# Kernel optimization log

Hardware: AMD Instinct MI355X
Metric: run time of the kernel (lower is better)

## Reference

```python
import jax, jax.numpy as jnp
import numpy as np

B, T, D = 4, 2048, 1024
H = 16
HD = D // H  # 64


def setup_inputs() -> dict:
    key = jax.random.key(0)
    ks = jax.random.split(key, 9)
    x = jax.random.normal(ks[0], (B, T, D), dtype=jnp.float32)
    s = 0.02
    Wq = jax.random.normal(ks[1], (D, D), dtype=jnp.float32) * s
    bq = jnp.zeros((D,), dtype=jnp.float32)
    Wk = jax.random.normal(ks[2], (D, D), dtype=jnp.float32) * s
    bk = jnp.zeros((D,), dtype=jnp.float32)
    Wv = jax.random.normal(ks[3], (D, D), dtype=jnp.float32) * s
    bv = jnp.zeros((D,), dtype=jnp.float32)
    Wo = jax.random.normal(ks[4], (D, D), dtype=jnp.float32) * s
    bo = jnp.zeros((D,), dtype=jnp.float32)
    return {"x": x, "Wq": Wq, "bq": bq, "Wk": Wk, "bk": bk,
            "Wv": Wv, "bv": bv, "Wo": Wo, "bo": bo}


def reference(x, Wq, bq, Wk, bk, Wv, bv, Wo, bo):
    Bn, Tn, Dn = x.shape
    # projections -> [B, H, T, HD]
    def split_heads(y):
        return y.reshape(Bn, Tn, H, HD).transpose(0, 2, 1, 3)
    Q = split_heads(x @ Wq + bq)
    K = split_heads(x @ Wk + bk)
    V = split_heads(x @ Wv + bv)
    scores = jnp.einsum('bhqd,bhkd->bhqk', Q, K) / jnp.sqrt(jnp.float32(HD))
    attn = jax.nn.softmax(scores, axis=-1)           # [B, H, T, T]
    attn_weights = attn.mean(axis=1)                 # [B, T, T] (head-averaged)
    out = jnp.einsum('bhqk,bhkd->bhqd', attn, V)     # [B, H, T, HD]
    out = out.transpose(0, 2, 1, 3).reshape(Bn, Tn, Dn)
    out = out @ Wo + bo                              # [B, T, D]
    # pooling weight: mean over query dim -> [B, 1, T] -> transpose -> [B, T, 1]
    pool_w = attn_weights.mean(axis=1, keepdims=True).transpose(0, 2, 1)
    pooled = (out * pool_w).sum(axis=1)              # [B, D]
    return pooled
```

## Files before the change

### kernel.cpp

```cpp
#include <hip/hip_runtime.h>
#include <hip/hip_bf16.h>
#include <stdint.h>

#define B_ 4
#define T_ 2048
#define D_ 1024
#define H_ 16
#define HD_ 64

#define QSCALE 0.1803368801111244f

typedef __bf16 bf16_t;
typedef __bf16 bf16x8 __attribute__((ext_vector_type(8)));
typedef __bf16 bf16x4 __attribute__((ext_vector_type(4)));
typedef float f32x4 __attribute__((ext_vector_type(4)));

__device__ __forceinline__ f32x4 mfma16(bf16x8 a, bf16x8 b, f32x4 c) {
  return __builtin_amdgcn_mfma_f32_16x16x32_bf16(a, b, c, 0, 0, 0);
}

__device__ __forceinline__ void gload_lds16(const bf16_t* g, bf16_t* l) {
  __builtin_amdgcn_global_load_lds(
      (const __attribute__((address_space(1))) unsigned int*)g,
      (__attribute__((address_space(3))) unsigned int*)l, 16, 0, 0);
}

__device__ __forceinline__ float exp2g(float x) {
  return __builtin_amdgcn_exp2f(x);
}

__global__ __launch_bounds__(256) void conv_x(const float* __restrict__ x,
                                              bf16_t* __restrict__ xb) {
  size_t i = ((size_t)blockIdx.x * 256 + threadIdx.x) * 8;
  float4 a = *(const float4*)(x + i);
  float4 b = *(const float4*)(x + i + 4);
  bf16x8 v;
  v[0] = (bf16_t)a.x; v[1] = (bf16_t)a.y; v[2] = (bf16_t)a.z; v[3] = (bf16_t)a.w;
  v[4] = (bf16_t)b.x; v[5] = (bf16_t)b.y; v[6] = (bf16_t)b.z; v[7] = (bf16_t)b.w;
  *(bf16x8*)(xb + i) = v;
}

__global__ __launch_bounds__(256) void conv_wt3(
    const float* __restrict__ Wq, const float* __restrict__ Wk,
    const float* __restrict__ Wv, bf16_t* __restrict__ WtAll) {
  __shared__ float Ls[64][65];
  const int tid = threadIdx.x;
  const int z = blockIdx.z;
  const float* W = (z == 0) ? Wq : (z == 1) ? Wk : Wv;
  bf16_t* Wt = WtAll + (size_t)z * 1024 * D_;
  const int k0 = blockIdx.y * 64, n0 = blockIdx.x * 64;
  const int rr = tid >> 4, cc = (tid & 15) * 4;
#pragma unroll
  for (int it = 0; it < 4; ++it) {
    int r = rr + it * 16;
    float4 v = *(const float4*)(W + (size_t)(k0 + r) * D_ + n0 + cc);
    Ls[r][cc] = v.x; Ls[r][cc + 1] = v.y; Ls[r][cc + 2] = v.z; Ls[r][cc + 3] = v.w;
  }
  __syncthreads();
#pragma unroll
  for (int it = 0; it < 4; ++it) {
    int nl = rr + it * 16;
    bf16x4 o;
    o[0] = (bf16_t)Ls[cc][nl];     o[1] = (bf16_t)Ls[cc + 1][nl];
    o[2] = (bf16_t)Ls[cc + 2][nl]; o[3] = (bf16_t)Ls[cc + 3][nl];
    *(bf16x4*)(Wt + (size_t)(n0 + nl) * D_ + k0 + cc) = o;
  }
}

__global__ __launch_bounds__(256) void gemm_qkv(
    const bf16_t* __restrict__ A, const bf16_t* __restrict__ Bt,
    const float* __restrict__ bq, const float* __restrict__ bk,
    const float* __restrict__ bv,
    bf16_t* __restrict__ Qo, bf16_t* __restrict__ Ko, bf16_t* __restrict__ Vo)
{
  __shared__ __align__(16) bf16_t As[128 * 64];
  __shared__ __align__(16) bf16_t Bs[128 * 64];
  const int tid = threadIdx.x, lane = tid & 63, wv = tid >> 6;
  const int wr = wv >> 1, wc = wv & 1;
  const int wg = blockIdx.x;
  const int xcd = wg & 7;
  const int local = wg >> 3;
  const int mb = xcd * 8 + (local & 7);
  const int nb = local >> 3;
  const int m0 = mb * 128, n0 = nb * 128;
  const int mode = nb >> 3;
  const int lr = lane & 15, lg = lane >> 4;
  const int srow = wv * 8 + (lane >> 3);
  const int scol = (lane & 7) * 8;

  f32x4 acc[4][4] = {};

  for (int k0 = 0; k0 < D_; k0 += 64) {
    __syncthreads();
#pragma unroll
    for (int i = 0; i < 4; ++i) {
      gload_lds16(A + (size_t)(m0 + i * 32 + srow) * D_ + k0 + scol,
                  &As[(i * 32 + wv * 8) * 64]);
      gload_lds16(Bt + (size_t)(n0 + i * 32 + srow) * D_ + k0 + scol,
                  &Bs[(i * 32 + wv * 8) * 64]);
    }
    __syncthreads();

#pragma unroll
    for (int ks = 0; ks < 2; ++ks) {
      bf16x8 af[4], bfr[4];
#pragma unroll
      for (int i = 0; i < 4; ++i)
        af[i] = *(const bf16x8*)&As[(wr * 64 + i * 16 + lr) * 64 + ks * 32 + lg * 8];
#pragma unroll
      for (int j = 0; j < 4; ++j)
        bfr[j] = *(const bf16x8*)&Bs[(wc * 64 + j * 16 + lr) * 64 + ks * 32 + lg * 8];
#pragma unroll
      for (int i = 0; i < 4; ++i)
#pragma unroll
        for (int j = 0; j < 4; ++j)
          acc[i][j] = mfma16(af[i], bfr[j], acc[i][j]);
    }
  }

  bf16_t* out = (mode == 0) ? Qo : (mode == 1) ? Ko : Vo;
  const float* bias = (mode == 0) ? bq : (mode == 1) ? bk : bv;
  const float scale = (mode == 0) ? QSCALE : 1.0f;
  const int nl0 = n0 - mode * 1024;
#pragma unroll
  for (int j = 0; j < 4; ++j) {
    int n = nl0 + wc * 64 + j * 16 + lr;
    float bval = bias[n];
    int h = n >> 6, d = n & 63;
#pragma unroll
    for (int i = 0; i < 4; ++i)
#pragma unroll
      for (int r = 0; r < 4; ++r) {
        int m = m0 + wr * 64 + i * 16 + lg * 4 + r;
        int b = m >> 11, t = m & (T_ - 1);
        float val = (acc[i][j][r] + bval) * scale;
        out[(((size_t)(b * H_ + h)) * T_ + t) * HD_ + d] = (bf16_t)val;
      }
  }
}

__global__ __launch_bounds__(256) void qkv_gemm_f32(
    const float* __restrict__ x, const float* __restrict__ W,
    const float* __restrict__ bias, bf16_t* __restrict__ out, float scale)
{
  __shared__ bf16_t As[128][40];
  __shared__ bf16_t Bs[128][40];
  const int tid = threadIdx.x, lane = tid & 63, wv = tid >> 6;
  const int wr = wv >> 1, wc = wv & 1;
  const int m0 = blockIdx.y * 128, n0 = blockIdx.x * 128;
  const int lr = lane & 15, lg = lane >> 4;
  f32x4 acc[4][4] = {};
  const int xr = tid >> 3, xc = tid & 7;
  const int wk = tid >> 5, wn = tid & 31;

  for (int k0 = 0; k0 < D_; k0 += 32) {
    __syncthreads();
#pragma unroll
    for (int it = 0; it < 4; ++it) {
      int r = xr + it * 32;
      float4 v = *(const float4*)(x + (size_t)(m0 + r) * D_ + k0 + xc * 4);
      bf16_t* dst = &As[r][xc * 4];
      dst[0] = (bf16_t)v.x; dst[1] = (bf16_t)v.y;
      dst[2] = (bf16_t)v.z; dst[3] = (bf16_t)v.w;
    }
#pragma unroll
    for (int it = 0; it < 4; ++it) {
      int k = wk + it * 8;
      float4 v = *(const float4*)(W + (size_t)(k0 + k) * D_ + n0 + wn * 4);
      Bs[wn * 4 + 0][k] = (bf16_t)v.x;
      Bs[wn * 4 + 1][k] = (bf16_t)v.y;
      Bs[wn * 4 + 2][k] = (bf16_t)v.z;
      Bs[wn * 4 + 3][k] = (bf16_t)v.w;
    }
    __syncthreads();
    bf16x8 af[4], bfr[4];
#pragma unroll
    for (int i = 0; i < 4; ++i) af[i]  = *(const bf16x8*)&As[wr * 64 + i * 16 + lr][lg * 8];
#pragma unroll
    for (int j = 0; j < 4; ++j) bfr[j] = *(const bf16x8*)&Bs[wc * 64 + j * 16 + lr][lg * 8];
#pragma unroll
    for (int i = 0; i < 4; ++i)
#pragma unroll
      for (int j = 0; j < 4; ++j)
        acc[i][j] = mfma16(af[i], bfr[j], acc[i][j]);
  }

#pragma unroll
  for (int j = 0; j < 4; ++j) {
    int n = n0 + wc * 64 + j * 16 + lr;
    float bval = bias[n];
    int h = n >> 6, d = n & 63;
#pragma unroll
    for (int i = 0; i < 4; ++i)
#pragma unroll
      for (int r = 0; r < 4; ++r) {
        int m = m0 + wr * 64 + i * 16 + lg * 4 + r;
        int b = m >> 11, t = m & (T_ - 1);
        float val = (acc[i][j][r] + bval) * scale;
        out[(((size_t)(b * H_ + h)) * T_ + t) * HD_ + d] = (bf16_t)val;
      }
  }
}

__global__ __launch_bounds__(256) void attn_rowsum(
    const bf16_t* __restrict__ Q, const bf16_t* __restrict__ K,
    float* __restrict__ Linv)
{
  const int tid = threadIdx.x, lane = tid & 63, wv = tid >> 6;
  const int lr = lane & 15, lg = lane >> 4;
  const int wg = blockIdx.x;
  const int p_ = wg >> 3;
  const int bh = (wg & 7) * 8 + (p_ >> 4);
  const int qc = p_ & 15;
  const int q0w = qc * 128 + wv * 32;

  const bf16_t* Qb = Q + (size_t)bh * T_ * HD_;
  const bf16_t* Kb = K + (size_t)bh * T_ * HD_;

  bf16x8 qa[2][2];
#pragma unroll
  for (int qq = 0; qq < 2; ++qq)
#pragma unroll
    for (int ks = 0; ks < 2; ++ks)
      qa[qq][ks] = *(const bf16x8*)(Qb + (size_t)(q0w + qq * 16 + lr) * HD_ +
                                    ks * 32 + lg * 8);

  float accl[2][4] = {};

  for (int tb = 0; tb < T_; tb += 64) {
#pragma unroll
    for (int ts = 0; ts < 4; ++ts) {
      const int t16 = tb + ts * 16;
      bf16x8 kb0 = *(const bf16x8*)(Kb + (size_t)(t16 + lr) * HD_ + lg * 8);
      bf16x8 kb1 = *(const bf16x8*)(Kb + (size_t)(t16 + lr) * HD_ + 32 + lg * 8);
#pragma unroll
      for (int qq = 0; qq < 2; ++qq) {
        f32x4 s = {};
        __builtin_amdgcn_s_setprio(1);
        s = mfma16(qa[qq][0], kb0, s);
        s = mfma16(qa[qq][1], kb1, s);
        __builtin_amdgcn_s_setprio(0);
#pragma unroll
        for (int r = 0; r < 4; ++r)
          accl[qq][r] += exp2g(s[r]);
      }
    }
  }

#pragma unroll
  for (int qq = 0; qq < 2; ++qq)
#pragma unroll
    for (int r = 0; r < 4; ++r) {
      float v = accl[qq][r];
      v += __shfl_xor(v, 1); v += __shfl_xor(v, 2);
      v += __shfl_xor(v, 4); v += __shfl_xor(v, 8);
      accl[qq][r] = v;
    }
  if (lr == 0) {
#pragma unroll
    for (int qq = 0; qq < 2; ++qq)
#pragma unroll
      for (int r = 0; r < 4; ++r)
        Linv[(size_t)bh * T_ + q0w + qq * 16 + lg * 4 + r] =
            1.f / accl[qq][r];
  }
}

__global__ __launch_bounds__(256) void attn_colsum(
    const bf16_t* __restrict__ Q, const bf16_t* __restrict__ K,
    const float* __restrict__ Linv, float* __restrict__ colsum)
{
  const int tid = threadIdx.x, lane = tid & 63, wv = tid >> 6;
  const int lr = lane & 15, lg = lane >> 4;
  const int wg = blockIdx.x;
  const int p_ = wg >> 3;
  const int bh = (wg & 7) * 8 + (p_ >> 4);
  const int rem = p_ & 15;
  const int tc = rem >> 1;
  const int qs = rem & 1;
  const int b = bh >> 4;
  const int t0w = tc * 256 + wv * 64;

  const bf16_t* Qb = Q + (size_t)bh * T_ * HD_;
  const bf16_t* Kb = K + (size_t)bh * T_ * HD_;
  const float* Lb = Linv + (size_t)bh * T_;

  bf16x8 kf[4][2];
#pragma unroll
  for (int tt = 0; tt < 4; ++tt)
#pragma unroll
    for (int ks = 0; ks < 2; ++ks)
      kf[tt][ks] = *(const bf16x8*)(Kb + (size_t)(t0w + tt * 16 + lr) * HD_ +
                                    ks * 32 + lg * 8);

  float acc[4][4] = {};

  const int qlo = qs * (T_ / 2), qhi = qlo + T_ / 2;
  for (int qb = qlo; qb < qhi; qb += 64) {
#pragma unroll
    for (int qt = 0; qt < 4; ++qt) {
      const int q = qb + qt * 16 + lr;
      bf16x8 qv0 = *(const bf16x8*)(Qb + (size_t)q * HD_ + lg * 8);
      bf16x8 qv1 = *(const bf16x8*)(Qb + (size_t)q * HD_ + 32 + lg * 8);
      const float lv = Lb[q];
#pragma unroll
      for (int tt = 0; tt < 4; ++tt) {
        f32x4 s = {};
        __builtin_amdgcn_s_setprio(1);
        s = mfma16(kf[tt][0], qv0, s);
        s = mfma16(kf[tt][1], qv1, s);
        __builtin_amdgcn_s_setprio(0);
#pragma unroll
        for (int r = 0; r < 4; ++r)
          acc[tt][r] = fmaf(exp2g(s[r]), lv, acc[tt][r]);
      }
    }
  }

#pragma unroll
  for (int tt = 0; tt < 4; ++tt)
#pragma unroll
    for (int r = 0; r < 4; ++r) {
      float v = acc[tt][r];
      v += __shfl_xor(v, 1); v += __shfl_xor(v, 2);
      v += __shfl_xor(v, 4); v += __shfl_xor(v, 8);
      acc[tt][r] = v;
    }
  if (lr == 0) {
#pragma unroll
    for (int tt = 0; tt < 4; ++tt)
#pragma unroll
      for (int r = 0; r < 4; ++r)
        atomicAdd(&colsum[b * T_ + t0w + tt * 16 + lg * 4 + r], acc[tt][r]);
  }
}

__global__ __launch_bounds__(256) void attn_w2(
    const bf16_t* __restrict__ Q, const bf16_t* __restrict__ K,
    const float* __restrict__ Linv, const float* __restrict__ CS,
    float* __restrict__ w2)
{
  const int tid = threadIdx.x, lane = tid & 63, wv = tid >> 6;
  const int lr = lane & 15, lg = lane >> 4;
  const int wg = blockIdx.x;
  const int p_ = wg >> 3;
  const int bh = (wg & 7) * 8 + (p_ >> 4);
  const int rem = p_ & 15;
  const int tc = rem >> 1;
  const int qs = rem & 1;
  const int b = bh >> 4;
  const int t0w = tc * 256 + wv * 64;

  const bf16_t* Qb = Q + (size_t)bh * T_ * HD_;
  const bf16_t* Kb = K + (size_t)bh * T_ * HD_;
  const float* Lb = Linv + (size_t)bh * T_;
  const float* Cb = CS + (size_t)b * T_;

  bf16x8 kf[4][2];
#pragma unroll
  for (int tt = 0; tt < 4; ++tt)
#pragma unroll
    for (int ks = 0; ks < 2; ++ks)
      kf[tt][ks] = *(const bf16x8*)(Kb + (size_t)(t0w + tt * 16 + lr) * HD_ +
                                    ks * 32 + lg * 8);

  float acc[4][4] = {};

  const int qlo = qs * (T_ / 2), qhi = qlo + T_ / 2;
  for (int qb = qlo; qb < qhi; qb += 64) {
#pragma unroll
    for (int qt = 0; qt < 4; ++qt) {
      const int q = qb + qt * 16 + lr;
      bf16x8 qv0 = *(const bf16x8*)(Qb + (size_t)q * HD_ + lg * 8);
      bf16x8 qv1 = *(const bf16x8*)(Qb + (size_t)q * HD_ + 32 + lg * 8);
      const float lv = Cb[q] * Lb[q] * (1.f / 32768.f);
#pragma unroll
      for (int tt = 0; tt < 4; ++tt) {
        f32x4 s = {};
        __builtin_amdgcn_s_setprio(1);
        s = mfma16(kf[tt][0], qv0, s);
        s = mfma16(kf[tt][1], qv1, s);
        __builtin_amdgcn_s_setprio(0);
#pragma unroll
        for (int r = 0; r < 4; ++r)
          acc[tt][r] = fmaf(exp2g(s[r]), lv, acc[tt][r]);
      }
    }
  }

#pragma unroll
  for (int tt = 0; tt < 4; ++tt)
#pragma unroll
    for (int r = 0; r < 4; ++r) {
      float v = acc[tt][r];
      v += __shfl_xor(v, 1); v += __shfl_xor(v, 2);
      v += __shfl_xor(v, 4); v += __shfl_xor(v, 8);
      acc[tt][r] = v;
    }
  if (lr == 0) {
#pragma unroll
    for (int tt = 0; tt < 4; ++tt)
#pragma unroll
      for (int r = 0; r < 4; ++r)
        atomicAdd(&w2[(size_t)bh * T_ + t0w + tt * 16 + lg * 4 + r],
                  acc[tt][r]);
  }
}

__global__ __launch_bounds__(256) void pool_wv(
    const bf16_t* __restrict__ V, const float* __restrict__ W2,
    float* __restrict__ pre)
{
  __shared__ float sm[256];
  const int wg = blockIdx.x;
  const int bh = wg >> 3, sc = wg & 7;
  const int b = bh >> 4, h = bh & 15;
  const int tid = threadIdx.x, d = tid & 63, tg = tid >> 6;
  const bf16_t* Vb = V + (size_t)bh * T_ * HD_ + (size_t)sc * 256 * HD_;
  const float* wb = W2 + (size_t)bh * T_ + sc * 256;
  float acc = 0.f;
  for (int s = tg; s < 256; s += 4)
    acc += wb[s] * (float)Vb[(size_t)s * HD_ + d];
  sm[tid] = acc;
  __syncthreads();
  if (tid < 64) {
    float s = sm[tid] + sm[tid + 64] + sm[tid + 128] + sm[tid + 192];
    atomicAdd(&pre[b * D_ + h * 64 + tid], s);
  }
}

__global__ __launch_bounds__(256) void out_acc(
    const float* __restrict__ pre, const float* __restrict__ Wo,
    const float* __restrict__ bo, float* __restrict__ out)
{
  const int dc = blockIdx.x & 3, kb = blockIdx.x >> 2;
  const int d = dc * 256 + threadIdx.x;
  const int k0 = kb * 32;
  float acc0 = 0.f, acc1 = 0.f, acc2 = 0.f, acc3 = 0.f;
#pragma unroll
  for (int kk = 0; kk < 32; ++kk) {
    const int k = k0 + kk;
    const float w = Wo[(size_t)k * D_ + d];
    acc0 = fmaf(pre[k],            w, acc0);
    acc1 = fmaf(pre[D_ + k],       w, acc1);
    acc2 = fmaf(pre[2 * D_ + k],   w, acc2);
    acc3 = fmaf(pre[3 * D_ + k],   w, acc3);
  }
  if (kb == 0) {
    const float bd = bo[d];
    acc0 += bd; acc1 += bd; acc2 += bd; acc3 += bd;
  }
  atomicAdd(&out[d],           acc0);
  atomicAdd(&out[D_ + d],      acc1);
  atomicAdd(&out[2 * D_ + d],  acc2);
  atomicAdd(&out[3 * D_ + d],  acc3);
}

extern "C" void kernel_launch(void* const* d_in, const int* in_sizes, int n_in,
                              void* d_out, int out_size, void* d_ws, size_t ws_size,
                              hipStream_t stream)
{
  (void)in_sizes; (void)n_in; (void)out_size;
  const float* x  = (const float*)d_in[0];
  const float* Wq = (const float*)d_in[1];
  const float* bq = (const float*)d_in[2];
  const float* Wk = (const float*)d_in[3];
  const float* bk = (const float*)d_in[4];
  const float* Wv = (const float*)d_in[5];
  const float* bv = (const float*)d_in[6];
  const float* Wo = (const float*)d_in[7];
  const float* bo = (const float*)d_in[8];
  float* out = (float*)d_out;

  char* ws = (char*)d_ws;
  const size_t MB = 1ull << 20;
  const size_t KB = 1024;
  bf16_t* Qw = (bf16_t*)(ws);
  bf16_t* Kw = (bf16_t*)(ws + 16 * MB);
  bf16_t* Vw = (bf16_t*)(ws + 32 * MB);
  bf16_t* XB = (bf16_t*)(ws + 48 * MB);
  const size_t need_fast = 72 * MB;
  const bool fast = ws_size >= need_fast;

  size_t soff = fast ? 70 * MB : 64 * MB;
  float* LV  = (float*)(ws + soff);
  float* CS  = (float*)(ws + soff + 512 * KB);
  float* PRE = (float*)(ws + soff + 544 * KB);
  float* W2  = (float*)(ws + soff + 560 * KB);
  dim3 blk(256, 1, 1);

  if (fast) {
    bf16_t* WtAll = (bf16_t*)(ws + 64 * MB);
    conv_x<<<dim3((B_ * T_ * D_) / (256 * 8), 1, 1), blk, 0, stream>>>(x, XB);
    conv_wt3<<<dim3(16, 16, 3), blk, 0, stream>>>(Wq, Wk, Wv, WtAll);
    gemm_qkv<<<dim3(1536, 1, 1), blk, 0, stream>>>(XB, WtAll, bq, bk, bv,
                                                   Qw, Kw, Vw);
  } else {
    qkv_gemm_f32<<<dim3(8, 64, 1), blk, 0, stream>>>(x, Wq, bq, Qw, QSCALE);
    qkv_gemm_f32<<<dim3(8, 64, 1), blk, 0, stream>>>(x, Wk, bk, Kw, 1.0f);
    qkv_gemm_f32<<<dim3(8, 64, 1), blk, 0, stream>>>(x, Wv, bv, Vw, 1.0f);
  }

  hipMemsetAsync(CS, 0, 560 * KB - 512 * KB + 512 * KB, stream);
  hipMemsetAsync(out, 0, (size_t)B_ * D_ * sizeof(float), stream);

  attn_rowsum<<<dim3(1024, 1, 1), blk, 0, stream>>>(Qw, Kw, LV);
  attn_colsum<<<dim3(1024, 1, 1), blk, 0, stream>>>(Qw, Kw, LV, CS);
  attn_w2<<<dim3(1024, 1, 1), blk, 0, stream>>>(Qw, Kw, LV, CS, W2);
  pool_wv<<<dim3(512, 1, 1), blk, 0, stream>>>(Vw, W2, PRE);
  out_acc<<<dim3(128, 1, 1), blk, 0, stream>>>(PRE, Wo, bo, out);
}
```

Measured before the change: 366.6 us.

## Enlarge per-wave tiles in attention passes and split rowsum over key halves

The rowsum kernel now gives each wave 64 query rows (instead of 32) and splits the key range in half across blocks. Partial sums are combined with atomics, and a new inv_l kernel takes the reciprocal afterwards. The colsum and w2 kernels give each wave 128 key rows (8 tiles) and split queries into quarters, which doubles register-held K reuse per Q load. The aim is to cut redundant global loads of K/Q per MFMA, at the cost of more registers, an extra launch, and more atomics.

```diff
diff --git a/kernel.cpp b/kernel.cpp
--- a/kernel.cpp
+++ b/kernel.cpp
@@ -204,71 +204,7 @@
 
 __global__ __launch_bounds__(256) void attn_rowsum(
     const bf16_t* __restrict__ Q, const bf16_t* __restrict__ K,
-    float* __restrict__ Linv)
-{
-  const int tid = threadIdx.x, lane = tid & 63, wv = tid >> 6;
-  const int lr = lane & 15, lg = lane >> 4;
-  const int wg = blockIdx.x;
-  const int p_ = wg >> 3;
-  const int bh = (wg & 7) * 8 + (p_ >> 4);
-  const int qc = p_ & 15;
-  const int q0w = qc * 128 + wv * 32;
-
-  const bf16_t* Qb = Q + (size_t)bh * T_ * HD_;
-  const bf16_t* Kb = K + (size_t)bh * T_ * HD_;
-
-  bf16x8 qa[2][2];
-#pragma unroll
-  for (int qq = 0; qq < 2; ++qq)
-#pragma unroll
-    for (int ks = 0; ks < 2; ++ks)
-      qa[qq][ks] = *(const bf16x8*)(Qb + (size_t)(q0w + qq * 16 + lr) * HD_ +
-                                    ks * 32 + lg * 8);
-
-  float accl[2][4] = {};
-
-  for (int tb = 0; tb < T_; tb += 64) {
-#pragma unroll
-    for (int ts = 0; ts < 4; ++ts) {
-      const int t16 = tb + ts * 16;
-      bf16x8 kb0 = *(const bf16x8*)(Kb + (size_t)(t16 + lr) * HD_ + lg * 8);
-      bf16x8 kb1 = *(const bf16x8*)(Kb + (size_t)(t16 + lr) * HD_ + 32 + lg * 8);
-#pragma unroll
-      for (int qq = 0; qq < 2; ++qq) {
-        f32x4 s = {};
-        __builtin_amdgcn_s_setprio(1);
-        s = mfma16(qa[qq][0], kb0, s);
-        s = mfma16(qa[qq][1], kb1, s);
-        __builtin_amdgcn_s_setprio(0);
-#pragma unroll
-        for (int r = 0; r < 4; ++r)
-          accl[qq][r] += exp2g(s[r]);
-      }
-    }
-  }
-
-#pragma unroll
-  for (int qq = 0; qq < 2; ++qq)
-#pragma unroll
-    for (int r = 0; r < 4; ++r) {
-      float v = accl[qq][r];
-      v += __shfl_xor(v, 1); v += __shfl_xor(v, 2);
-      v += __shfl_xor(v, 4); v += __shfl_xor(v, 8);
-      accl[qq][r] = v;
-    }
-  if (lr == 0) {
-#pragma unroll
-    for (int qq = 0; qq < 2; ++qq)
-#pragma unroll
-      for (int r = 0; r < 4; ++r)
-        Linv[(size_t)bh * T_ + q0w + qq * 16 + lg * 4 + r] =
-            1.f / accl[qq][r];
-  }
-}
-
-__global__ __launch_bounds__(256) void attn_colsum(
-    const bf16_t* __restrict__ Q, const bf16_t* __restrict__ K,
-    const float* __restrict__ Linv, float* __restrict__ colsum)
+    float* __restrict__ Lsum)
 {
   const int tid = threadIdx.x, lane = tid & 63, wv = tid >> 6;
   const int lr = lane & 15, lg = lane >> 4;
@@ -276,69 +212,73 @@
   const int p_ = wg >> 3;
   const int bh = (wg & 7) * 8 + (p_ >> 4);
   const int rem = p_ & 15;
-  const int tc = rem >> 1;
-  const int qs = rem & 1;
-  const int b = bh >> 4;
-  const int t0w = tc * 256 + wv * 64;
+  const int qc = rem >> 1;
+  const int th = rem & 1;
+  const int q0w = qc * 256 + wv * 64;
 
   const bf16_t* Qb = Q + (size_t)bh * T_ * HD_;
   const bf16_t* Kb = K + (size_t)bh * T_ * HD_;
-  const float* Lb = Linv + (size_t)bh * T_;
-
-  bf16x8 kf[4][2];
-#pragma unroll
-  for (int tt = 0; tt < 4; ++tt)
+
+  bf16x8 qa[4][2];
+#pragma unroll
+  for (int qq = 0; qq < 4; ++qq)
 #pragma unroll
     for (int ks = 0; ks < 2; ++ks)
-      kf[tt][ks] = *(const bf16x8*)(Kb + (size_t)(t0w + tt * 16 + lr) * HD_ +
+      qa[qq][ks] = *(const bf16x8*)(Qb + (size_t)(q0w + qq * 16 + lr) * HD_ +
                                     ks * 32 + lg * 8);
 
   float acc[4][4] = {};
 
-  const int qlo = qs * (T_ / 2), qhi = qlo + T_ / 2;
-  for (int qb = qlo; qb < qhi; qb += 64) {
-#pragma unroll
-    for (int qt = 0; qt < 4; ++qt) {
-      const int q = qb + qt * 16 + lr;
-      bf16x8 qv0 = *(const bf16x8*)(Qb + (size_t)q * HD_ + lg * 8);
-      bf16x8 qv1 = *(const bf16x8*)(Qb + (size_t)q * HD_ + 32 + lg * 8);
-      const float lv = Lb[q];
-#pragma unroll
-      for (int tt = 0; tt < 4; ++tt) {
+  const int tlo = th * (T_ / 2), thi = tlo + T_ / 2;
+  for (int tb = tlo; tb < thi; tb += 64) {
+#pragma unroll
+    for (int ts = 0; ts < 4; ++ts) {
+      const int t16 = tb + ts * 16;
+      bf16x8 kb0 = *(const bf16x8*)(Kb + (size_t)(t16 + lr) * HD_ + lg * 8);
+      bf16x8 kb1 = *(const bf16x8*)(Kb + (size_t)(t16 + lr) * HD_ + 32 + lg * 8);
+#pragma unroll
+      for (int qq = 0; qq < 4; ++qq) {
         f32x4 s = {};
         __builtin_amdgcn_s_setprio(1);
-        s = mfma16(kf[tt][0], qv0, s);
-        s = mfma16(kf[tt][1], qv1, s);
+        s = mfma16(qa[qq][0], kb0, s);
+        s = mfma16(qa[qq][1], kb1, s);
         __builtin_amdgcn_s_setprio(0);
 #pragma unroll
         for (int r = 0; r < 4; ++r)
-          acc[tt][r] = fmaf(exp2g(s[r]), lv, acc[tt][r]);
+          acc[qq][r] += exp2g(s[r]);
       }
     }
   }
 
 #pragma unroll
-  for (int tt = 0; tt < 4; ++tt)
+  for (int qq = 0; qq < 4; ++qq)
 #pragma unroll
     for (int r = 0; r < 4; ++r) {
-      float v = acc[tt][r];
+      float v = acc[qq][r];
       v += __shfl_xor(v, 1); v += __shfl_xor(v, 2);
       v += __shfl_xor(v, 4); v += __shfl_xor(v, 8);
-      acc[tt][r] = v;
+      acc[qq][r] = v;
     }
   if (lr == 0) {
 #pragma unroll
-    for (int tt = 0; tt < 4; ++tt)
+    for (int qq = 0; qq < 4; ++qq)
 #pragma unroll
       for (int r = 0; r < 4; ++r)
-        atomicAdd(&colsum[b * T_ + t0w + tt * 16 + lg * 4 + r], acc[tt][r]);
-  }
-}
-
-__global__ __launch_bounds__(256) void attn_w2(
+        atomicAdd(&Lsum[(size_t)bh * T_ + q0w + qq * 16 + lg * 4 + r],
+                  acc[qq][r]);
+  }
+}
+
+__global__ __launch_bounds__(256) void inv_l(float* __restrict__ L) {
+  size_t i = ((size_t)blockIdx.x * 256 + threadIdx.x) * 4;
+  float4 v = *(float4*)(L + i);
+  v.x = 1.f / v.x; v.y = 1.f / v.y; v.z = 1.f / v.z; v.w = 1.f / v.w;
+  *(float4*)(L + i) = v;
+}
+
+__global__ __launch_bounds__(256) void attn_colsum(
     const bf16_t* __restrict__ Q, const bf16_t* __restrict__ K,
-    const float* __restrict__ Linv, const float* __restrict__ CS,
-    float* __restrict__ w2)
+    const float* __restrict__ Linv, float* __restrict__ colsum)
 {
   const int tid = threadIdx.x, lane = tid & 63, wv = tid >> 6;
   const int lr = lane & 15, lg = lane >> 4;
@@ -346,27 +286,97 @@
   const int p_ = wg >> 3;
   const int bh = (wg & 7) * 8 + (p_ >> 4);
   const int rem = p_ & 15;
-  const int tc = rem >> 1;
-  const int qs = rem & 1;
+  const int tc = rem >> 2;
+  const int qs = rem & 3;
   const int b = bh >> 4;
-  const int t0w = tc * 256 + wv * 64;
+  const int t0w = tc * 512 + wv * 128;
+
+  const bf16_t* Qb = Q + (size_t)bh * T_ * HD_;
+  const bf16_t* Kb = K + (size_t)bh * T_ * HD_;
+  const float* Lb = Linv + (size_t)bh * T_;
+
+  bf16x8 kf[8][2];
+#pragma unroll
+  for (int tt = 0; tt < 8; ++tt)
+#pragma unroll
+    for (int ks = 0; ks < 2; ++ks)
+      kf[tt][ks] = *(const bf16x8*)(Kb + (size_t)(t0w + tt * 16 + lr) * HD_ +
+                                    ks * 32 + lg * 8);
+
+  float acc[8][4] = {};
+
+  const int qlo = qs * (T_ / 4), qhi = qlo + T_ / 4;
+  for (int qb = qlo; qb < qhi; qb += 64) {
+#pragma unroll
+    for (int qt = 0; qt < 4; ++qt) {
+      const int q = qb + qt * 16 + lr;
+      bf16x8 qv0 = *(const bf16x8*)(Qb + (size_t)q * HD_ + lg * 8);
+      bf16x8 qv1 = *(const bf16x8*)(Qb + (size_t)q * HD_ + 32 + lg * 8);
+      const float lv = Lb[q];
+#pragma unroll
+      for (int tt = 0; tt < 8; ++tt) {
+        f32x4 s = {};
+        __builtin_amdgcn_s_setprio(1);
+        s = mfma16(kf[tt][0], qv0, s);
+        s = mfma16(kf[tt][1], qv1, s);
+        __builtin_amdgcn_s_setprio(0);
+#pragma unroll
+        for (int r = 0; r < 4; ++r)
+          acc[tt][r] = fmaf(exp2g(s[r]), lv, acc[tt][r]);
+      }
+    }
+  }
+
+#pragma unroll
+  for (int tt = 0; tt < 8; ++tt)
+#pragma unroll
+    for (int r = 0; r < 4; ++r) {
+      float v = acc[tt][r];
+      v += __shfl_xor(v, 1); v += __shfl_xor(v, 2);
+      v += __shfl_xor(v, 4); v += __shfl_xor(v, 8);
+      acc[tt][r] = v;
+    }
+  if (lr == 0) {
+#pragma unroll
+    for (int tt = 0; tt < 8; ++tt)
+#pragma unroll
+      for (int r = 0; r < 4; ++r)
+        atomicAdd(&colsum[b * T_ + t0w + tt * 16 + lg * 4 + r], acc[tt][r]);
+  }
+}
+
+__global__ __launch_bounds__(256) void attn_w2(
+    const bf16_t* __restrict__ Q, const bf16_t* __restrict__ K,
+    const float* __restrict__ Linv, const float* __restrict__ CS,
+    float* __restrict__ w2)
+{
+  const int tid = threadIdx.x, lane = tid & 63, wv = tid >> 6;
+  const int lr = lane & 15, lg = lane >> 4;
+  const int wg = blockIdx.x;
+  const int p_ = wg >> 3;
+  const int bh = (wg & 7) * 8 + (p_ >> 4);
+  const int rem = p_ & 15;
+  const int tc = rem >> 2;
+  const int qs = rem & 3;
+  const int b = bh >> 4;
+  const int t0w = tc * 512 + wv * 128;
 
   const bf16_t* Qb = Q + (size_t)bh * T_ * HD_;
   const bf16_t* Kb = K + (size_t)bh * T_ * HD_;
   const float* Lb = Linv + (size_t)bh * T_;
   const float* Cb = CS + (size_t)b * T_;
 
-  bf16x8 kf[4][2];
-#pragma unroll
-  for (int tt = 0; tt < 4; ++tt)
+  bf16x8 kf[8][2];
+#pragma unroll
+  for (int tt = 0; tt < 8; ++tt)
 #pragma unroll
     for (int ks = 0; ks < 2; ++ks)
       kf[tt][ks] = *(const bf16x8*)(Kb + (size_t)(t0w + tt * 16 + lr) * HD_ +
                                     ks * 32 + lg * 8);
 
-  float acc[4][4] = {};
-
-  const int qlo = qs * (T_ / 2), qhi = qlo + T_ / 2;
+  float acc[8][4] = {};
+
+  const int qlo = qs * (T_ / 4), qhi = qlo + T_ / 4;
   for (int qb = qlo; qb < qhi; qb += 64) {
 #pragma unroll
     for (int qt = 0; qt < 4; ++qt) {
@@ -375,7 +385,7 @@
       bf16x8 qv1 = *(const bf16x8*)(Qb + (size_t)q * HD_ + 32 + lg * 8);
       const float lv = Cb[q] * Lb[q] * (1.f / 32768.f);
 #pragma unroll
-      for (int tt = 0; tt < 4; ++tt) {
+      for (int tt = 0; tt < 8; ++tt) {
         f32x4 s = {};
         __builtin_amdgcn_s_setprio(1);
         s = mfma16(kf[tt][0], qv0, s);
@@ -389,7 +399,7 @@
   }
 
 #pragma unroll
-  for (int tt = 0; tt < 4; ++tt)
+  for (int tt = 0; tt < 8; ++tt)
 #pragma unroll
     for (int r = 0; r < 4; ++r) {
       float v = acc[tt][r];
@@ -399,7 +409,7 @@
     }
   if (lr == 0) {
 #pragma unroll
-    for (int tt = 0; tt < 4; ++tt)
+    for (int tt = 0; tt < 8; ++tt)
 #pragma unroll
       for (int r = 0; r < 4; ++r)
         atomicAdd(&w2[(size_t)bh * T_ + t0w + tt * 16 + lg * 4 + r],
@@ -501,10 +511,11 @@
     qkv_gemm_f32<<<dim3(8, 64, 1), blk, 0, stream>>>(x, Wv, bv, Vw, 1.0f);
   }
 
-  hipMemsetAsync(CS, 0, 560 * KB - 512 * KB + 512 * KB, stream);
+  hipMemsetAsync(LV, 0, 1072 * KB, stream);
   hipMemsetAsync(out, 0, (size_t)B_ * D_ * sizeof(float), stream);
 
   attn_rowsum<<<dim3(1024, 1, 1), blk, 0, stream>>>(Qw, Kw, LV);
+  inv_l<<<dim3((B_ * H_ * T_) / (256 * 4), 1, 1), blk, 0, stream>>>(LV);
   attn_colsum<<<dim3(1024, 1, 1), blk, 0, stream>>>(Qw, Kw, LV, CS);
   attn_w2<<<dim3(1024, 1, 1), blk, 0, stream>>>(Qw, Kw, LV, CS, W2);
   pool_wv<<<dim3(512, 1, 1), blk, 0, stream>>>(Vw, W2, PRE);
```

New measurement: 308.9 us. 15.7% less time.
